# Kernel tuning notes

Measured on AMD Instinct MI355X. Metric: run time of the kernel, lower is better.

The kernel has to match this reference:

```python
import jax, jax.numpy as jnp
import numpy as np

N_NODES = 100000
N_EDGES = 1600000
IN_FEATS = 128
H_FEATS = 64


def setup_inputs() -> dict:
    key = jax.random.key(0)
    ks = jax.random.split(key, 6)
    x = jax.random.normal(ks[0], (N_NODES, IN_FEATS), dtype=jnp.float32)
    # xavier-normal-ish scaling for weights
    W1 = jax.random.normal(ks[1], (IN_FEATS, 2 * H_FEATS), dtype=jnp.float32) * (1.414 * (2.0 / (IN_FEATS + 2 * H_FEATS)) ** 0.5)
    b1 = jnp.zeros((2 * H_FEATS,), dtype=jnp.float32)
    W2 = jax.random.normal(ks[2], (2 * H_FEATS, H_FEATS), dtype=jnp.float32) * (1.414 * (2.0 / (2 * H_FEATS + H_FEATS)) ** 0.5)
    b2 = jnp.zeros((H_FEATS,), dtype=jnp.float32)
    src = jax.random.randint(ks[3], (N_EDGES,), 0, N_NODES, dtype=jnp.int64 if jax.config.jax_enable_x64 else jnp.int32)
    dst = jax.random.randint(ks[4], (N_EDGES,), 0, N_NODES, dtype=jnp.int64 if jax.config.jax_enable_x64 else jnp.int32)
    return {"x": x, "W1": W1, "b1": b1, "W2": W2, "b2": b2, "src": src, "dst": dst}


def _graph_conv(x, W, b, src, dst, n_nodes):
    # DGL GraphConv with norm='both': h = D_dst^{-1/2} A D_src^{-1/2} x W + b
    ones = jnp.ones((src.shape[0],), dtype=x.dtype)
    deg_out = jax.ops.segment_sum(ones, src, num_segments=n_nodes)  # out-degree of src
    deg_in = jax.ops.segment_sum(ones, dst, num_segments=n_nodes)   # in-degree of dst
    norm_out = jnp.where(deg_out > 0, jax.lax.rsqrt(jnp.maximum(deg_out, 1.0)), 0.0)
    norm_in = jnp.where(deg_in > 0, jax.lax.rsqrt(jnp.maximum(deg_in, 1.0)), 0.0)
    h = x * norm_out[:, None]
    # multiply by W first (in_feats >= out_feats here), mathematically identical
    h = h @ W
    msgs = h[src]                                   # [E, out] gather
    agg = jax.ops.segment_sum(msgs, dst, num_segments=n_nodes)  # [N, out] scatter-add
    return agg * norm_in[:, None] + b


def reference(x, W1, b1, W2, b2, src, dst):
    n = x.shape[0]
    h = jax.nn.relu(_graph_conv(x, W1, b1, src, dst, n))
    h = jax.nn.relu(_graph_conv(h, W2, b2, src, dst, n))
    return h
```

## Files before the change

### kernel.cpp

```cpp
#include <hip/hip_runtime.h>
#include <hip/hip_bf16.h>

#define INF 128
#define HF 64

#define HS 64
#define HR_H 32768
#define NR_H 4
#define HR_F 16384
#define NR_F 7

typedef __attribute__((ext_vector_type(8))) short short8v;
typedef __attribute__((ext_vector_type(4))) float f32x4;

__device__ inline unsigned short bf16r(float f) {
    __hip_bfloat16 h = __float2bfloat16(f);
    return *reinterpret_cast<unsigned short*>(&h);
}

__global__ __launch_bounds__(512) void hist2_kernel(const int* __restrict__ src,
        const int* __restrict__ dst, unsigned* __restrict__ Hs,
        unsigned* __restrict__ Hd, int E, int SL) {
    __shared__ unsigned h[HR_H / 2];
    const int t = threadIdx.x;
    const int which = blockIdx.x >> 8;
    const int rs = blockIdx.x & 255;
    const int r = rs >> 6;
    const int s = rs & 63;
    const int base = r * HR_H;
    const int* key = which ? dst : src;
    unsigned* H = which ? Hd : Hs;
    for (int i = t; i < HR_H / 2; i += 512) h[i] = 0u;
    __syncthreads();
    const int e0 = s * SL;
    const int e1 = min(e0 + SL, E);
    const int nq = (e1 > e0) ? (e1 - e0) >> 2 : 0;
    for (int g = t; g < nq; g += 512) {
        int4 k4 = *reinterpret_cast<const int4*>(key + e0 + 4 * g);
        unsigned v0 = (unsigned)(k4.x - base);
        unsigned v1 = (unsigned)(k4.y - base);
        unsigned v2 = (unsigned)(k4.z - base);
        unsigned v3 = (unsigned)(k4.w - base);
        if (v0 < HR_H) atomicAdd(&h[v0 >> 1], 1u << ((v0 & 1) << 4));
        if (v1 < HR_H) atomicAdd(&h[v1 >> 1], 1u << ((v1 & 1) << 4));
        if (v2 < HR_H) atomicAdd(&h[v2 >> 1], 1u << ((v2 & 1) << 4));
        if (v3 < HR_H) atomicAdd(&h[v3 >> 1], 1u << ((v3 & 1) << 4));
    }
    for (int e = e0 + 4 * nq + t; e < e1; e += 512) {
        unsigned v = (unsigned)(key[e] - base);
        if (v < HR_H) atomicAdd(&h[v >> 1], 1u << ((v & 1) << 4));
    }
    __syncthreads();
    unsigned* Hp = H + (size_t)(r * HS + s) * (HR_H / 2);
    for (int i = t; i < HR_H / 2; i += 512) Hp[i] = h[i];
}

__global__ __launch_bounds__(256) void prep_kernel(const unsigned* __restrict__ Hs,
        unsigned* __restrict__ Hd, int* __restrict__ cnt_dst,
        float* __restrict__ nout, float* __restrict__ nin, int N) {
    int w = blockIdx.x * 256 + threadIdx.x;
    int NW = (N + 1) >> 1;
    if (w >= NW) return;
    int r  = w >> 14;
    int lw = w & 16383;
    const unsigned* ps = Hs + (size_t)r * HS * (HR_H / 2) + lw;
    unsigned s_lo = 0, s_hi = 0;
    #pragma unroll 8
    for (int s = 0; s < HS; ++s) {
        unsigned v = ps[(size_t)s * (HR_H / 2)];
        s_lo += v & 0xffffu;
        s_hi += v >> 16;
    }
    unsigned* pd = Hd + (size_t)r * HS * (HR_H / 2) + lw;
    unsigned run_lo = 0, run_hi = 0;
    for (int s = 0; s < HS; ++s) {
        unsigned v = pd[(size_t)s * (HR_H / 2)];
        pd[(size_t)s * (HR_H / 2)] = run_lo | (run_hi << 16);
        run_lo += v & 0xffffu;
        run_hi += v >> 16;
    }
    int n0 = 2 * w, n1 = 2 * w + 1;
    cnt_dst[n0] = (int)run_lo;
    nout[n0] = s_lo ? rsqrtf((float)s_lo) : 0.f;
    nin[n0]  = run_lo ? rsqrtf((float)run_lo) : 0.f;
    if (n1 < N) {
        cnt_dst[n1] = (int)run_hi;
        nout[n1] = s_hi ? rsqrtf((float)s_hi) : 0.f;
        nin[n1]  = run_hi ? rsqrtf((float)run_hi) : 0.f;
    }
}

__global__ __launch_bounds__(256) void scan_blocks_kernel(const int* __restrict__ deg,
        int* __restrict__ rowstart, int* __restrict__ bsum, int N) {
    __shared__ int sh[256];
    const int b = blockIdx.x, t = threadIdx.x;
    const int base = b * 1024 + t * 4;
    int v0 = (base + 0 < N) ? deg[base + 0] : 0;
    int v1 = (base + 1 < N) ? deg[base + 1] : 0;
    int v2 = (base + 2 < N) ? deg[base + 2] : 0;
    int v3 = (base + 3 < N) ? deg[base + 3] : 0;
    sh[t] = v0 + v1 + v2 + v3;
    __syncthreads();
    for (int off = 1; off < 256; off <<= 1) {
        int x = (t >= off) ? sh[t - off] : 0;
        __syncthreads();
        sh[t] += x;
        __syncthreads();
    }
    if (t == 255) bsum[b] = sh[255];
    int run = (t == 0) ? 0 : sh[t - 1];
    if (base + 0 < N) { rowstart[base + 0] = run; run += v0; }
    if (base + 1 < N) { rowstart[base + 1] = run; run += v1; }
    if (base + 2 < N) { rowstart[base + 2] = run; run += v2; }
    if (base + 3 < N) { rowstart[base + 3] = run; }
}

__global__ __launch_bounds__(1024) void scan_bsums_kernel(int* __restrict__ bsum, int NB) {
    __shared__ int sh[1024];
    const int t = threadIdx.x;
    int v = (t < NB) ? bsum[t] : 0;
    sh[t] = v;
    __syncthreads();
    for (int off = 1; off < 1024; off <<= 1) {
        int x = (t >= off) ? sh[t - off] : 0;
        __syncthreads();
        sh[t] += x;
        __syncthreads();
    }
    if (t < NB) bsum[t] = sh[t] - v;
}

__global__ __launch_bounds__(256) void scan_add_kernel(int* __restrict__ rowstart,
        const int* __restrict__ bsum, int N) {
    const int b = blockIdx.x;
    if (b == 0) return;
    const int t = threadIdx.x;
    const int off = bsum[b];
    const int base = b * 1024 + t * 4;
    if (base + 0 < N) rowstart[base + 0] += off;
    if (base + 1 < N) rowstart[base + 1] += off;
    if (base + 2 < N) rowstart[base + 2] += off;
    if (base + 3 < N) rowstart[base + 3] += off;
}

__global__ __launch_bounds__(512) void fillp_kernel(const int* __restrict__ src,
        const int* __restrict__ dst, const int* __restrict__ rowstart,
        const unsigned* __restrict__ Hd, int* __restrict__ esrc, int E, int N, int SL) {
    __shared__ int h[HR_F];
    const int t = threadIdx.x;
    const int r = blockIdx.x >> 6;
    const int s = blockIdx.x & 63;
    const int base = r * HR_F;
    const int rh   = r >> 1;
    const int off0 = (r & 1) * HR_F;
    const unsigned* Hp = Hd + (size_t)(rh * HS + s) * (HR_H / 2);
    for (int i = t; i < HR_F; i += 512) {
        int n = base + i;
        int seed = 0;
        if (n < N) {
            int l = off0 + i;
            unsigned v = Hp[l >> 1];
            unsigned pre = (l & 1) ? (v >> 16) : (v & 0xffffu);
            seed = rowstart[n] + (int)pre;
        }
        h[i] = seed;
    }
    __syncthreads();
    const int e0 = s * SL;
    const int e1 = min(e0 + SL, E);
    const int nq = (e1 > e0) ? (e1 - e0) >> 2 : 0;
    for (int g = t; g < nq; g += 512) {
        const int e = e0 + 4 * g;
        int4 d4 = *reinterpret_cast<const int4*>(dst + e);
        int4 s4 = *reinterpret_cast<const int4*>(src + e);
        unsigned v0 = (unsigned)(d4.x - base);
        unsigned v1 = (unsigned)(d4.y - base);
        unsigned v2 = (unsigned)(d4.z - base);
        unsigned v3 = (unsigned)(d4.w - base);
        if (v0 < HR_F) esrc[atomicAdd(&h[v0], 1)] = s4.x;
        if (v1 < HR_F) esrc[atomicAdd(&h[v1], 1)] = s4.y;
        if (v2 < HR_F) esrc[atomicAdd(&h[v2], 1)] = s4.z;
        if (v3 < HR_F) esrc[atomicAdd(&h[v3], 1)] = s4.w;
    }
    for (int e = e0 + 4 * nq + t; e < e1; e += 512) {
        unsigned v = (unsigned)(dst[e] - base);
        if (v < HR_F) esrc[atomicAdd(&h[v], 1)] = src[e];
    }
}

__global__ __launch_bounds__(256) void wt_kernel(const float* __restrict__ W1,
        const float* __restrict__ W2, unsigned short* __restrict__ W1T,
        unsigned short* __restrict__ W2T) {
    int i = blockIdx.x * 256 + threadIdx.x;
    if (i < 128 * 128) {
        int o = i >> 7, k = i & 127;
        W1T[i] = bf16r(W1[k * 128 + o]);
    }
    if (i < 64 * 128) {
        int o = i >> 7, k = i & 127;
        W2T[i] = bf16r(W2[k * 64 + o]);
    }
}

template<int OUT, bool BF16IN>
__global__ __launch_bounds__(256) void gemm_mfma_kernel(const void* __restrict__ Xv,
        const float* __restrict__ rowscale,
        const unsigned short* __restrict__ WT,
        unsigned short* __restrict__ H, int N) {
    constexpr int K   = 128;
    constexpr int LDP = K + 8;
    constexpr int NT  = OUT / 16;

    __shared__ unsigned short sX[64 * LDP];
    __shared__ unsigned short sWT[OUT * LDP];

    const int tid  = threadIdx.x;
    const int row0 = blockIdx.x * 64;

    if constexpr (BF16IN) {
        const unsigned short* X = (const unsigned short*)Xv;
        for (int i = tid; i < 64 * 16; i += 256) {
            int rr = i >> 4, kq = i & 15;
            int gr = row0 + rr;
            int4 u = make_int4(0, 0, 0, 0);
            if (gr < N)
                u = *reinterpret_cast<const int4*>(&X[(size_t)gr * K + kq * 8]);
            *reinterpret_cast<int4*>(&sX[rr * LDP + kq * 8]) = u;
        }
    } else {
        const float* X = (const float*)Xv;
        for (int i = tid; i < 64 * 32; i += 256) {
            int rr = i >> 5, kq = i & 31;
            int gr = row0 + rr;
            float4 v = make_float4(0.f, 0.f, 0.f, 0.f);
            if (gr < N) {
                v = reinterpret_cast<const float4*>(X)[(size_t)gr * 32 + kq];
                if (rowscale) { float s = rowscale[gr]; v.x *= s; v.y *= s; v.z *= s; v.w *= s; }
            }
            ushort4 u;
            u.x = bf16r(v.x); u.y = bf16r(v.y); u.z = bf16r(v.z); u.w = bf16r(v.w);
            *reinterpret_cast<ushort4*>(&sX[rr * LDP + kq * 4]) = u;
        }
    }
    for (int i = tid; i < OUT * (K / 8); i += 256) {
        int o = i >> 4, kq = i & 15;
        *reinterpret_cast<int4*>(&sWT[o * LDP + kq * 8]) =
            *reinterpret_cast<const int4*>(&WT[o * K + kq * 8]);
    }
    __syncthreads();

    const int w  = tid >> 6;
    const int l  = tid & 63;
    const int lr = l & 15;
    const int lk = (l >> 4) * 8;

    f32x4 acc[NT];
    #pragma unroll
    for (int n = 0; n < NT; ++n) acc[n] = (f32x4){0.f, 0.f, 0.f, 0.f};

    #pragma unroll
    for (int k0 = 0; k0 < K; k0 += 32) {
        short8v a = *reinterpret_cast<const short8v*>(&sX[(w * 16 + lr) * LDP + k0 + lk]);
        #pragma unroll
        for (int n = 0; n < NT; ++n) {
            short8v b = *reinterpret_cast<const short8v*>(&sWT[(n * 16 + lr) * LDP + k0 + lk]);
            acc[n] = __builtin_amdgcn_mfma_f32_16x16x32_bf16(a, b, acc[n], 0, 0, 0);
        }
    }

    const int rbase = row0 + w * 16 + (l >> 4) * 4;
    #pragma unroll
    for (int j = 0; j < 4; ++j) {
        int gr = rbase + j;
        if (gr < N) {
            #pragma unroll
            for (int n = 0; n < NT; ++n)
                H[(size_t)gr * OUT + n * 16 + lr] = bf16r(acc[n][j]);
        }
    }
}


__global__ __launch_bounds__(256) void agg128_kernel(const __hip_bfloat162* __restrict__ H,
        const int* __restrict__ esrc, const int* __restrict__ rowstart,
        const int* __restrict__ cnt,
        const float* __restrict__ nin, const float* __restrict__ bias,
        const float* __restrict__ nout, unsigned int* __restrict__ outb, int N) {
    int wid  = (blockIdx.x * 256 + threadIdx.x) >> 6;
    int lane = threadIdx.x & 63;
    if (wid >= N) return;
    int beg = rowstart[wid];
    int cw  = cnt[wid];
    float2 a0 = make_float2(0.f, 0.f), a1 = make_float2(0.f, 0.f);
    float2 a2 = make_float2(0.f, 0.f), a3 = make_float2(0.f, 0.f);
    float2 a4 = make_float2(0.f, 0.f), a5 = make_float2(0.f, 0.f);
    float2 a6 = make_float2(0.f, 0.f), a7 = make_float2(0.f, 0.f);
    for (int j0 = 0; j0 < cw; j0 += 64) {
        int m = min(64, cw - j0);
        int idx = (lane < m) ? esrc[beg + j0 + lane] : 0;
        int jj = 0;
        for (; jj + 8 <= m; jj += 8) {
            int s0 = __shfl(idx, jj + 0);
            int s1 = __shfl(idx, jj + 1);
            int s2 = __shfl(idx, jj + 2);
            int s3 = __shfl(idx, jj + 3);
            int s4 = __shfl(idx, jj + 4);
            int s5 = __shfl(idx, jj + 5);
            int s6 = __shfl(idx, jj + 6);
            int s7 = __shfl(idx, jj + 7);
            float2 v0 = __bfloat1622float2(H[(size_t)s0 * 64 + lane]);
            float2 v1 = __bfloat1622float2(H[(size_t)s1 * 64 + lane]);
            float2 v2 = __bfloat1622float2(H[(size_t)s2 * 64 + lane]);
            float2 v3 = __bfloat1622float2(H[(size_t)s3 * 64 + lane]);
            float2 v4 = __bfloat1622float2(H[(size_t)s4 * 64 + lane]);
            float2 v5 = __bfloat1622float2(H[(size_t)s5 * 64 + lane]);
            float2 v6 = __bfloat1622float2(H[(size_t)s6 * 64 + lane]);
            float2 v7 = __bfloat1622float2(H[(size_t)s7 * 64 + lane]);
            a0.x += v0.x; a0.y += v0.y;  a1.x += v1.x; a1.y += v1.y;
            a2.x += v2.x; a2.y += v2.y;  a3.x += v3.x; a3.y += v3.y;
            a4.x += v4.x; a4.y += v4.y;  a5.x += v5.x; a5.y += v5.y;
            a6.x += v6.x; a6.y += v6.y;  a7.x += v7.x; a7.y += v7.y;
        }
        for (; jj < m; ++jj) {
            int s0 = __shfl(idx, jj);
            float2 v0 = __bfloat1622float2(H[(size_t)s0 * 64 + lane]);
            a0.x += v0.x; a0.y += v0.y;
        }
    }
    a0.x += a1.x + a2.x + a3.x + a4.x + a5.x + a6.x + a7.x;
    a0.y += a1.y + a2.y + a3.y + a4.y + a5.y + a6.y + a7.y;
    float s = nin[wid];
    float2 b = ((const float2*)bias)[lane];
    float r0 = fmaxf(fmaf(a0.x, s, b.x), 0.f);
    float r1 = fmaxf(fmaf(a0.y, s, b.y), 0.f);
    float t = nout[wid];
    r0 *= t; r1 *= t;
    __hip_bfloat162 p = __float22bfloat162_rn(make_float2(r0, r1));
    outb[(size_t)wid * 64 + lane] = *reinterpret_cast<unsigned int*>(&p);
}

__global__ __launch_bounds__(256) void agg64_kernel(const __hip_bfloat16* __restrict__ H,
        const int* __restrict__ esrc, const int* __restrict__ rowstart,
        const int* __restrict__ cnt,
        const float* __restrict__ nin, const float* __restrict__ bias,
        float* __restrict__ out, int N) {
    int wid  = (blockIdx.x * 256 + threadIdx.x) >> 6;
    int lane = threadIdx.x & 63;
    if (wid >= N) return;
    int beg = rowstart[wid];
    int cw  = cnt[wid];
    float a0 = 0.f, a1 = 0.f, a2 = 0.f, a3 = 0.f;
    float a4 = 0.f, a5 = 0.f, a6 = 0.f, a7 = 0.f;
    for (int j0 = 0; j0 < cw; j0 += 64) {
        int m = min(64, cw - j0);
        int idx = (lane < m) ? esrc[beg + j0 + lane] : 0;
        int jj = 0;
        for (; jj + 8 <= m; jj += 8) {
            int s0 = __shfl(idx, jj + 0);
            int s1 = __shfl(idx, jj + 1);
            int s2 = __shfl(idx, jj + 2);
            int s3 = __shfl(idx, jj + 3);
            int s4 = __shfl(idx, jj + 4);
            int s5 = __shfl(idx, jj + 5);
            int s6 = __shfl(idx, jj + 6);
            int s7 = __shfl(idx, jj + 7);
            a0 += __bfloat162float(H[(size_t)s0 * 64 + lane]);
            a1 += __bfloat162float(H[(size_t)s1 * 64 + lane]);
            a2 += __bfloat162float(H[(size_t)s2 * 64 + lane]);
            a3 += __bfloat162float(H[(size_t)s3 * 64 + lane]);
            a4 += __bfloat162float(H[(size_t)s4 * 64 + lane]);
            a5 += __bfloat162float(H[(size_t)s5 * 64 + lane]);
            a6 += __bfloat162float(H[(size_t)s6 * 64 + lane]);
            a7 += __bfloat162float(H[(size_t)s7 * 64 + lane]);
        }
        for (; jj < m; ++jj) {
            int s0 = __shfl(idx, jj);
            a0 += __bfloat162float(H[(size_t)s0 * 64 + lane]);
        }
    }
    float acc = ((a0 + a1) + (a2 + a3)) + ((a4 + a5) + (a6 + a7));
    float r = fmaxf(fmaf(acc, nin[wid], bias[lane]), 0.f);
    out[(size_t)wid * 64 + lane] = r;
}


extern "C" void kernel_launch(void* const* d_in, const int* in_sizes, int n_in,
                              void* d_out, int out_size, void* d_ws, size_t ws_size,
                              hipStream_t stream) {
    const float* x  = (const float*)d_in[0];
    const float* W1 = (const float*)d_in[1];
    const float* b1 = (const float*)d_in[2];
    const float* W2 = (const float*)d_in[3];
    const float* b2 = (const float*)d_in[4];
    const int*   src = (const int*)d_in[5];
    const int*   dst = (const int*)d_in[6];

    const int N = in_sizes[0] / INF;
    const int E = in_sizes[5];

    char* ws = (char*)d_ws;
    const size_t padN    = (((size_t)N * 4 + 255) / 256) * 256;
    const size_t padE    = (((size_t)E * 4 + 255) / 256) * 256;
    const size_t HPbytes = (size_t)NR_H * HS * (HR_H / 2) * sizeof(unsigned);
    const size_t padAbf  = (((size_t)N * INF * 2 + 255) / 256) * 256;
    const size_t padWT   = 49152;

    float* out = (float*)d_out;

    int*   cnt_dst  = (int*)  (ws);
    int*   rowstart = (int*)  (ws + padN);
    float* nout     = (float*)(ws + 2 * padN);
    float* nin      = (float*)(ws + 3 * padN);
    int*   bsum     = (int*)  (ws + 4 * padN);
    unsigned short* W1T = (unsigned short*)(ws + 5 * padN);
    unsigned short* W2T = (unsigned short*)(ws + 5 * padN + 32768);
    int*   esrc     = (int*)  (ws + 5 * padN + padWT);
    char*  regionA  = ws + 5 * padN + padWT + padE;
    unsigned short* Bbf = (unsigned short*)(regionA + padAbf);
    unsigned* Hpart_dst = (unsigned*)(regionA + padAbf + padAbf);

    unsigned* Hpart_src = (unsigned*)regionA;
    unsigned short* Abf = (unsigned short*)regionA;

    const int NB = (N + 1023) / 1024;
    const int NW = (N + 1) >> 1;
    const int SL = ((((E + HS - 1) / HS) + 3) / 4) * 4;

    wt_kernel<<<64, 256, 0, stream>>>(W1, W2, W1T, W2T);

    hist2_kernel<<<2 * NR_H * HS, 512, 0, stream>>>(src, dst, Hpart_src, Hpart_dst, E, SL);

    prep_kernel<<<(NW + 255) / 256, 256, 0, stream>>>(Hpart_src, Hpart_dst,
                                                      cnt_dst, nout, nin, N);

    scan_blocks_kernel<<<NB, 256, 0, stream>>>(cnt_dst, rowstart, bsum, N);
    scan_bsums_kernel<<<1, 1024, 0, stream>>>(bsum, NB);
    scan_add_kernel<<<NB, 256, 0, stream>>>(rowstart, bsum, N);

    fillp_kernel<<<NR_F * HS, 512, 0, stream>>>(src, dst, rowstart, Hpart_dst, esrc, E, N, SL);

    const int GB = (N + 63) / 64;

    gemm_mfma_kernel<128, false><<<GB, 256, 0, stream>>>(x, nout, W1T, Abf, N);
    agg128_kernel<<<(N * 64 + 255) / 256, 256, 0, stream>>>(
        (const __hip_bfloat162*)Abf, esrc, rowstart, cnt_dst, nin, b1, nout,
        (unsigned int*)Bbf, N);

    gemm_mfma_kernel<64, true><<<GB, 256, 0, stream>>>(Bbf, nullptr, W2T, Abf, N);
    agg64_kernel<<<(N * 64 + 255) / 256, 256, 0, stream>>>(
        (const __hip_bfloat16*)Abf, esrc, rowstart, cnt_dst, nin, b2, out, N);
}
```

Baseline: 226.4 us.

## Store GEMM output in column-sliced layout and aggregate per 16-column slice

The GEMM now writes H as column slices of 16 bf16 values per node, slice-major, so each slice of the feature table is a compact N×32-byte array. The aggregation kernels are replaced by one templated kernel where each block handles one slice for a chunk of nodes. Each wave processes 8 neighbours at once with 8 lanes per neighbour and reduces with xor shuffles. The goal is to shrink the working set per slice so random gathers hit L2/MALL better, and to cut per-edge instruction overhead. The costs are extra esrc/rowstart reads per slice, cross-lane reductions, and output stores from only 8 lanes.

```diff
diff --git a/kernel.cpp b/kernel.cpp
--- a/kernel.cpp
+++ b/kernel.cpp
@@ -275,112 +275,79 @@
         if (gr < N) {
             #pragma unroll
             for (int n = 0; n < NT; ++n)
-                H[(size_t)gr * OUT + n * 16 + lr] = bf16r(acc[n][j]);
-        }
-    }
-}
-
-
-__global__ __launch_bounds__(256) void agg128_kernel(const __hip_bfloat162* __restrict__ H,
+                H[((size_t)n * N + gr) * 16 + lr] = bf16r(acc[n][j]);
+        }
+    }
+}
+
+template<bool L1>
+__global__ __launch_bounds__(256) void aggs_kernel(const __hip_bfloat162* __restrict__ Hs,
         const int* __restrict__ esrc, const int* __restrict__ rowstart,
-        const int* __restrict__ cnt,
-        const float* __restrict__ nin, const float* __restrict__ bias,
-        const float* __restrict__ nout, unsigned int* __restrict__ outb, int N) {
-    int wid  = (blockIdx.x * 256 + threadIdx.x) >> 6;
-    int lane = threadIdx.x & 63;
-    if (wid >= N) return;
-    int beg = rowstart[wid];
-    int cw  = cnt[wid];
-    float2 a0 = make_float2(0.f, 0.f), a1 = make_float2(0.f, 0.f);
-    float2 a2 = make_float2(0.f, 0.f), a3 = make_float2(0.f, 0.f);
-    float2 a4 = make_float2(0.f, 0.f), a5 = make_float2(0.f, 0.f);
-    float2 a6 = make_float2(0.f, 0.f), a7 = make_float2(0.f, 0.f);
-    for (int j0 = 0; j0 < cw; j0 += 64) {
-        int m = min(64, cw - j0);
-        int idx = (lane < m) ? esrc[beg + j0 + lane] : 0;
-        int jj = 0;
-        for (; jj + 8 <= m; jj += 8) {
-            int s0 = __shfl(idx, jj + 0);
-            int s1 = __shfl(idx, jj + 1);
-            int s2 = __shfl(idx, jj + 2);
-            int s3 = __shfl(idx, jj + 3);
-            int s4 = __shfl(idx, jj + 4);
-            int s5 = __shfl(idx, jj + 5);
-            int s6 = __shfl(idx, jj + 6);
-            int s7 = __shfl(idx, jj + 7);
-            float2 v0 = __bfloat1622float2(H[(size_t)s0 * 64 + lane]);
-            float2 v1 = __bfloat1622float2(H[(size_t)s1 * 64 + lane]);
-            float2 v2 = __bfloat1622float2(H[(size_t)s2 * 64 + lane]);
-            float2 v3 = __bfloat1622float2(H[(size_t)s3 * 64 + lane]);
-            float2 v4 = __bfloat1622float2(H[(size_t)s4 * 64 + lane]);
-            float2 v5 = __bfloat1622float2(H[(size_t)s5 * 64 + lane]);
-            float2 v6 = __bfloat1622float2(H[(size_t)s6 * 64 + lane]);
-            float2 v7 = __bfloat1622float2(H[(size_t)s7 * 64 + lane]);
-            a0.x += v0.x; a0.y += v0.y;  a1.x += v1.x; a1.y += v1.y;
-            a2.x += v2.x; a2.y += v2.y;  a3.x += v3.x; a3.y += v3.y;
-            a4.x += v4.x; a4.y += v4.y;  a5.x += v5.x; a5.y += v5.y;
-            a6.x += v6.x; a6.y += v6.y;  a7.x += v7.x; a7.y += v7.y;
-        }
-        for (; jj < m; ++jj) {
-            int s0 = __shfl(idx, jj);
-            float2 v0 = __bfloat1622float2(H[(size_t)s0 * 64 + lane]);
-            a0.x += v0.x; a0.y += v0.y;
-        }
-    }
-    a0.x += a1.x + a2.x + a3.x + a4.x + a5.x + a6.x + a7.x;
-    a0.y += a1.y + a2.y + a3.y + a4.y + a5.y + a6.y + a7.y;
-    float s = nin[wid];
-    float2 b = ((const float2*)bias)[lane];
-    float r0 = fmaxf(fmaf(a0.x, s, b.x), 0.f);
-    float r1 = fmaxf(fmaf(a0.y, s, b.y), 0.f);
-    float t = nout[wid];
-    r0 *= t; r1 *= t;
-    __hip_bfloat162 p = __float22bfloat162_rn(make_float2(r0, r1));
-    outb[(size_t)wid * 64 + lane] = *reinterpret_cast<unsigned int*>(&p);
-}
-
-__global__ __launch_bounds__(256) void agg64_kernel(const __hip_bfloat16* __restrict__ H,
-        const int* __restrict__ esrc, const int* __restrict__ rowstart,
-        const int* __restrict__ cnt,
-        const float* __restrict__ nin, const float* __restrict__ bias,
-        float* __restrict__ out, int N) {
-    int wid  = (blockIdx.x * 256 + threadIdx.x) >> 6;
-    int lane = threadIdx.x & 63;
-    if (wid >= N) return;
-    int beg = rowstart[wid];
-    int cw  = cnt[wid];
-    float a0 = 0.f, a1 = 0.f, a2 = 0.f, a3 = 0.f;
-    float a4 = 0.f, a5 = 0.f, a6 = 0.f, a7 = 0.f;
-    for (int j0 = 0; j0 < cw; j0 += 64) {
-        int m = min(64, cw - j0);
-        int idx = (lane < m) ? esrc[beg + j0 + lane] : 0;
-        int jj = 0;
-        for (; jj + 8 <= m; jj += 8) {
-            int s0 = __shfl(idx, jj + 0);
-            int s1 = __shfl(idx, jj + 1);
-            int s2 = __shfl(idx, jj + 2);
-            int s3 = __shfl(idx, jj + 3);
-            int s4 = __shfl(idx, jj + 4);
-            int s5 = __shfl(idx, jj + 5);
-            int s6 = __shfl(idx, jj + 6);
-            int s7 = __shfl(idx, jj + 7);
-            a0 += __bfloat162float(H[(size_t)s0 * 64 + lane]);
-            a1 += __bfloat162float(H[(size_t)s1 * 64 + lane]);
-            a2 += __bfloat162float(H[(size_t)s2 * 64 + lane]);
-            a3 += __bfloat162float(H[(size_t)s3 * 64 + lane]);
-            a4 += __bfloat162float(H[(size_t)s4 * 64 + lane]);
-            a5 += __bfloat162float(H[(size_t)s5 * 64 + lane]);
-            a6 += __bfloat162float(H[(size_t)s6 * 64 + lane]);
-            a7 += __bfloat162float(H[(size_t)s7 * 64 + lane]);
-        }
-        for (; jj < m; ++jj) {
-            int s0 = __shfl(idx, jj);
-            a0 += __bfloat162float(H[(size_t)s0 * 64 + lane]);
-        }
-    }
-    float acc = ((a0 + a1) + (a2 + a3)) + ((a4 + a5) + (a6 + a7));
-    float r = fmaxf(fmaf(acc, nin[wid], bias[lane]), 0.f);
-    out[(size_t)wid * 64 + lane] = r;
+        const int* __restrict__ cnt, const float* __restrict__ nin,
+        const float* __restrict__ bias, const float* __restrict__ nout,
+        void* __restrict__ outv, int N) {
+    constexpr int NSL = L1 ? 8 : 4;
+    const int bid = blockIdx.x;
+    const int slice = bid & (NSL - 1);
+    const int chunk = bid / NSL;
+    const int wv = threadIdx.x >> 6;
+    const int l  = threadIdx.x & 63;
+    const int g  = l >> 3;
+    const int f  = l & 7;
+    const __hip_bfloat162* T = Hs + (size_t)slice * N * 8;
+    const int colp = slice * 8 + f;
+    const int node0 = (chunk * 4 + wv) * 8;
+    for (int ni = 0; ni < 8; ++ni) {
+        int wid = node0 + ni;
+        if (wid >= N) return;
+        int beg = rowstart[wid];
+        int cw  = cnt[wid];
+        float ax = 0.f, ay = 0.f, bx = 0.f, by = 0.f;
+        for (int j0 = 0; j0 < cw; j0 += 64) {
+            int m = min(64, cw - j0);
+            int idx = (l < m) ? esrc[beg + j0 + l] : 0;
+            int jj = 0;
+            for (; jj + 16 <= m; jj += 16) {
+                int s0 = __shfl(idx, jj + g);
+                int s1 = __shfl(idx, jj + 8 + g);
+                float2 v0 = __bfloat1622float2(T[(size_t)s0 * 8 + f]);
+                float2 v1 = __bfloat1622float2(T[(size_t)s1 * 8 + f]);
+                ax += v0.x; ay += v0.y; bx += v1.x; by += v1.y;
+            }
+            if (jj + 8 <= m) {
+                int s0 = __shfl(idx, jj + g);
+                float2 v0 = __bfloat1622float2(T[(size_t)s0 * 8 + f]);
+                ax += v0.x; ay += v0.y;
+                jj += 8;
+            }
+            int rem = m - jj;
+            if (rem > 0) {
+                int s0 = __shfl(idx, jj + (g < rem ? g : 0));
+                if (g < rem) {
+                    float2 v0 = __bfloat1622float2(T[(size_t)s0 * 8 + f]);
+                    ax += v0.x; ay += v0.y;
+                }
+            }
+        }
+        ax += bx; ay += by;
+        ax += __shfl_xor(ax, 8);  ay += __shfl_xor(ay, 8);
+        ax += __shfl_xor(ax, 16); ay += __shfl_xor(ay, 16);
+        ax += __shfl_xor(ax, 32); ay += __shfl_xor(ay, 32);
+        if (g == 0) {
+            float s = nin[wid];
+            float2 b = ((const float2*)bias)[colp];
+            float r0 = fmaxf(fmaf(ax, s, b.x), 0.f);
+            float r1 = fmaxf(fmaf(ay, s, b.y), 0.f);
+            if constexpr (L1) {
+                float t = nout[wid];
+                r0 *= t; r1 *= t;
+                __hip_bfloat162 p = __float22bfloat162_rn(make_float2(r0, r1));
+                ((unsigned*)outv)[(size_t)wid * 64 + colp] = *reinterpret_cast<unsigned*>(&p);
+            } else {
+                ((float2*)outv)[(size_t)wid * 32 + colp] = make_float2(r0, r1);
+            }
+        }
+    }
 }
 
 
@@ -401,7 +368,6 @@
     char* ws = (char*)d_ws;
     const size_t padN    = (((size_t)N * 4 + 255) / 256) * 256;
     const size_t padE    = (((size_t)E * 4 + 255) / 256) * 256;
-    const size_t HPbytes = (size_t)NR_H * HS * (HR_H / 2) * sizeof(unsigned);
     const size_t padAbf  = (((size_t)N * INF * 2 + 255) / 256) * 256;
     const size_t padWT   = 49152;
 
@@ -440,13 +406,15 @@
     fillp_kernel<<<NR_F * HS, 512, 0, stream>>>(src, dst, rowstart, Hpart_dst, esrc, E, N, SL);
 
     const int GB = (N + 63) / 64;
+    const int CH = (N + 31) / 32;
 
     gemm_mfma_kernel<128, false><<<GB, 256, 0, stream>>>(x, nout, W1T, Abf, N);
-    agg128_kernel<<<(N * 64 + 255) / 256, 256, 0, stream>>>(
+    aggs_kernel<true><<<CH * 8, 256, 0, stream>>>(
         (const __hip_bfloat162*)Abf, esrc, rowstart, cnt_dst, nin, b1, nout,
-        (unsigned int*)Bbf, N);
+        (void*)Bbf, N);
 
     gemm_mfma_kernel<64, true><<<GB, 256, 0, stream>>>(Bbf, nullptr, W2T, Abf, N);
-    agg64_kernel<<<(N * 64 + 255) / 256, 256, 0, stream>>>(
-        (const __hip_bfloat16*)Abf, esrc, rowstart, cnt_dst, nin, b2, out, N);
-}
+    aggs_kernel<false><<<CH * 4, 256, 0, stream>>>(
+        (const __hip_bfloat162*)Abf, esrc, rowstart, cnt_dst, nin, b2, nullptr,
+        (void*)out, N);
+}
```

New measurement: 428.9 us. 89.4% more time.
